# Performance work log

Measured on AMD Instinct MI355X. Metric: run time of the kernel, lower is better.

Reference implementation:

```python
import jax, jax.numpy as jnp
import numpy as np


def postorder_positions(depth):
    """Post-order index of each node in a perfect binary tree of given depth.
    Returns dict: level -> np.array of post-order indices for the left-to-right
    nodes at that level (level 0 = leaves, level `depth` = root)."""
    levels = {0: np.array([0], dtype=np.int64)}
    size = 1  # size of depth-(d-1) subtree
    for d in range(1, depth + 1):
        new = {l: np.concatenate([levels[l], levels[l] + size]) for l in range(d)}
        new[d] = np.array([2 * size], dtype=np.int64)
        levels = new
        size = 2 * size + 1
    return levels


def setup_inputs() -> dict:
    key = jax.random.key(0)
    k1, k2, k3, k4, k5, k6 = jax.random.split(key, 6)
    VOCAB, E, LBL, LEAVES = 50000, 100, 2, 131072  # 2**17 leaves
    word_ids = jax.random.randint(k1, (LEAVES,), 0, VOCAB, dtype=jnp.int32)
    emb_table = jax.random.normal(k2, (VOCAB, E), dtype=jnp.float32) * 0.1
    Wl = jax.random.normal(k3, (E, E), dtype=jnp.float32) * 0.1
    bl = jax.random.normal(k4, (E,), dtype=jnp.float32) * 0.1
    Wp = jax.random.normal(k5, (LBL, E), dtype=jnp.float32) * 0.1
    bp = jax.random.normal(k6, (LBL,), dtype=jnp.float32) * 0.1
    return {"word_ids": word_ids, "emb_table": emb_table, "Wl": Wl, "bl": bl, "Wp": Wp, "bp": bp}


def reference(word_ids, emb_table, Wl, bl, Wp, bp):
    # Perfect binary tree, batched level-by-level (same math as the per-node
    # Python recursion in the torch module). NOTE: original uses fcl for BOTH
    # children, so internal node = relu(fcl(left) + fcl(right)).
    L = word_ids.shape[0]
    D = int(round(np.log2(L)))
    pos = postorder_positions(D)
    n_nodes = 2 * L - 1

    h = emb_table[word_ids]  # [L, E] leaf states
    out = jnp.zeros((n_nodes, 1, bp.shape[0]), dtype=h.dtype)
    for lvl in range(D + 1):
        proj = h @ Wp.T + bp                     # [n_lvl, label]
        out = out.at[jnp.asarray(pos[lvl])].set(proj[:, None, :])
        if lvl < D:
            # fcl(left)+fcl(right) = (left+right) @ Wl^T + 2*bl, then relu
            h = jax.nn.relu((h[0::2] + h[1::2]) @ Wl.T + 2.0 * bl)
    return out  # [n_nodes, 1, label] in post-order, matching torch.cat(node_list)
```

## Files before the change

kernel.cpp:

```cpp
#include <hip/hip_runtime.h>

typedef _Float16 h8v __attribute__((ext_vector_type(8)));
typedef float f4v __attribute__((ext_vector_type(4)));

#define RS 136
#define SD 68

__device__ __forceinline__ unsigned pk2f(float a, float b) {
  unsigned short ha = __builtin_bit_cast(unsigned short, (_Float16)a);
  unsigned short hb = __builtin_bit_cast(unsigned short, (_Float16)b);
  return (unsigned)ha | ((unsigned)hb << 16);
}
__device__ __forceinline__ float2 upk(unsigned u) {
  _Float16 lo = __builtin_bit_cast(_Float16, (unsigned short)(u & 0xffffu));
  _Float16 hi = __builtin_bit_cast(_Float16, (unsigned short)(u >> 16));
  return make_float2((float)lo, (float)hi);
}

__global__ void prep_kernel(const float* __restrict__ Wl,
                            unsigned short* __restrict__ Wlf) {
  int i = blockIdx.x * 256 + threadIdx.x;
  if (i < 128 * 128) {
    int o = i >> 7, k = i & 127;
    _Float16 v = (_Float16)0.f;
    if (o < 100 && k < 100) v = (_Float16)Wl[o * 100 + k];
    Wlf[i] = __builtin_bit_cast(unsigned short, v);
  }
}

__device__ __forceinline__ void load_bfrags(
    const unsigned short* __restrict__ Wlf, const float* __restrict__ bl,
    h8v (&B0)[4], h8v (&B1)[4], float& bias0, float& bias1,
    int wave, int quad, int c16) {
  int col0 = wave * 32 + c16;
  int col1 = col0 + 16;
  bias0 = (col0 < 100) ? 2.0f * bl[col0] : 0.f;
  bias1 = (col1 < 100) ? 2.0f * bl[col1] : 0.f;
  const _Float16* w0 = (const _Float16*)Wlf + col0 * 128 + quad * 8;
  const _Float16* w1 = (const _Float16*)Wlf + col1 * 128 + quad * 8;
  B0[0] = *(const h8v*)(w0);      B0[1] = *(const h8v*)(w0 + 32);
  B0[2] = *(const h8v*)(w0 + 64); B0[3] = *(const h8v*)(w0 + 96);
  B1[0] = *(const h8v*)(w1);      B1[1] = *(const h8v*)(w1 + 32);
  B1[2] = *(const h8v*)(w1 + 64); B1[3] = *(const h8v*)(w1 + 96);
}

__device__ __forceinline__ void mfma_level(
    const _Float16* srcE, const _Float16* srcO, bool pairMode,
    _Float16* dstE, _Float16* dstO, int nOut,
    const h8v (&B0)[4], const h8v (&B1)[4], float bias0, float bias1,
    int lane, int wave) {
  const int quad = lane >> 4, c16 = lane & 15;
  const int col0 = wave * 32 + c16, col1 = col0 + 16;
  const int tiles = (nOut + 15) >> 4;
  for (int rt = 0; rt < tiles; ++rt) {
    const int r = rt * 16 + c16;
    const h8v* pe = (const h8v*)(srcE + (size_t)r * RS + quad * 8);
    h8v A0, A1, A2, A3;
    if (pairMode) {
      const h8v* po = (const h8v*)(srcO + (size_t)r * RS + quad * 8);
      A0 = pe[0] + po[0];  A1 = pe[4] + po[4];
      A2 = pe[8] + po[8];  A3 = pe[12] + po[12];
    } else {
      A0 = pe[0]; A1 = pe[4]; A2 = pe[8]; A3 = pe[12];
    }
    f4v a0 = {bias0, bias0, bias0, bias0};
    f4v a1 = {bias1, bias1, bias1, bias1};
    a0 = __builtin_amdgcn_mfma_f32_16x16x32_f16(A0, B0[0], a0, 0, 0, 0);
    a0 = __builtin_amdgcn_mfma_f32_16x16x32_f16(A1, B0[1], a0, 0, 0, 0);
    a0 = __builtin_amdgcn_mfma_f32_16x16x32_f16(A2, B0[2], a0, 0, 0, 0);
    a0 = __builtin_amdgcn_mfma_f32_16x16x32_f16(A3, B0[3], a0, 0, 0, 0);
    a1 = __builtin_amdgcn_mfma_f32_16x16x32_f16(A0, B1[0], a1, 0, 0, 0);
    a1 = __builtin_amdgcn_mfma_f32_16x16x32_f16(A1, B1[1], a1, 0, 0, 0);
    a1 = __builtin_amdgcn_mfma_f32_16x16x32_f16(A2, B1[2], a1, 0, 0, 0);
    a1 = __builtin_amdgcn_mfma_f32_16x16x32_f16(A3, B1[3], a1, 0, 0, 0);
    #pragma unroll
    for (int rg = 0; rg < 4; ++rg) {
      int row = rt * 16 + quad * 4 + rg;
      _Float16* dr = ((row & 1) ? dstO : dstE) + (size_t)(row >> 1) * RS;
      dr[col0] = (_Float16)fmaxf(a0[rg], 0.f);
      dr[col1] = (_Float16)fmaxf(a1[rg], 0.f);
    }
  }
}

__device__ __forceinline__ void proj_rows(
    const _Float16* E, const _Float16* O, int nRows, const float* WpS,
    float bp0, float bp1, int lvl, long gbase, float* __restrict__ out, int tid) {
  if (tid >= nRows) return;
  const unsigned* row = (const unsigned*)((tid & 1) ? O : E) + (size_t)(tid >> 1) * SD;
  float q0 = bp0, q1 = bp1;
  #pragma unroll
  for (int p = 0; p < 25; ++p) {
    uint2 u = ((const uint2*)row)[p];
    float2 a = upk(u.x), b = upk(u.y);
    q0 = fmaf(a.x, WpS[4*p], fmaf(a.y, WpS[4*p+1],
         fmaf(b.x, WpS[4*p+2], fmaf(b.y, WpS[4*p+3], q0))));
    q1 = fmaf(a.x, WpS[100+4*p], fmaf(a.y, WpS[100+4*p+1],
         fmaf(b.x, WpS[100+4*p+2], fmaf(b.y, WpS[100+4*p+3], q1))));
  }
  long g = gbase + tid;
  long pos = ((g + 1) << (lvl + 1)) - 2 - __popc((unsigned)g);
  out[2 * pos] = q0; out[2 * pos + 1] = q1;
}

__device__ void tree_phase(
    const unsigned* __restrict__ src, unsigned* __restrict__ hdst,
    _Float16* Ea, _Float16* Oa, _Float16* Eb, _Float16* Ob,
    const float* WpS, float bp0, float bp1,
    const h8v (&B0)[4], const h8v (&B1)[4], float bias0, float bias1,
    float* __restrict__ out, int firstLvl, int nLvl, int nIn, int finalProj,
    long blk, int tid, int lane, int wave) {
  {
    unsigned* Ed = (unsigned*)Ea; unsigned* Od = (unsigned*)Oa;
    for (int i = tid; i < 64 * 64; i += 256) {
      int r = i >> 6, d = i & 63;
      unsigned val = (r < nIn && d < 50) ? src[(size_t)r * 50 + d] : 0u;
      ((r & 1) ? Od : Ed)[(r >> 1) * SD + d] = val;
    }
    unsigned* Ed2 = (unsigned*)Eb; unsigned* Od2 = (unsigned*)Ob;
    for (int i = tid; i < 32 * 64; i += 256) {
      int r = i >> 6, d = i & 63;
      ((r & 1) ? Od2 : Ed2)[(r >> 1) * SD + d] = 0u;
    }
  }
  __syncthreads();
  _Float16 *sE = Ea, *sO = Oa, *dE = Eb, *dO = Ob;
  int n = nIn >> 1;
  for (int p = 0; p < nLvl; ++p) {
    mfma_level(sE, sO, true, dE, dO, n, B0, B1, bias0, bias1, lane, wave);
    proj_rows(sE, sO, n * 2, WpS, bp0, bp1, firstLvl + p - 1,
              blk * (n * 2), out, tid);
    __syncthreads();
    _Float16* t;
    t = sE; sE = dE; dE = t;
    t = sO; sO = dO; dO = t;
    n >>= 1;
  }
  int R = nIn >> nLvl;
  if (finalProj)
    proj_rows(sE, sO, R, WpS, bp0, bp1, firstLvl + nLvl - 1, blk * R, out, tid);
  if (hdst) {
    for (int i = tid; i < R * 50; i += 256) {
      int r = i / 50, d = i % 50;
      hdst[(size_t)blk * R * 50 + i] =
          ((const unsigned*)((r & 1) ? sO : sE))[(r >> 1) * SD + d];
    }
  }
  __syncthreads();
}

__global__ __launch_bounds__(256, 4) void mega_kernel(
    const int* __restrict__ word_ids, const float* __restrict__ emb,
    const unsigned short* __restrict__ Wlf, const float* __restrict__ bl,
    const float* __restrict__ Wp, const float* __restrict__ bp,
    unsigned* __restrict__ h7g, unsigned* __restrict__ h13g,
    unsigned* __restrict__ cnts, float* __restrict__ out) {
  __shared__ _Float16 S1[64 * RS];
  __shared__ _Float16 Ea[32 * RS], Oa[32 * RS];
  __shared__ float WpS[200];
  __shared__ int claimS;
  _Float16* const Eb = S1;
  _Float16* const Ob = S1 + 16 * RS;

  const int tid = threadIdx.x, lane = tid & 63;
  const int wave = __builtin_amdgcn_readfirstlane(tid >> 6);
  const int quad = lane >> 4, c16 = lane & 15;
  const int blk = blockIdx.x;

  if (tid < 200) WpS[tid] = Wp[tid];
  {
    unsigned* S1d = (unsigned*)S1;
    for (int i = tid; i < 64 * 14; i += 256) S1d[(i / 14) * SD + 50 + (i % 14)] = 0;
  }
  const float bp0 = bp[0], bp1 = bp[1];

  const int l = tid >> 1, hh = tid & 1;
  const long gL = (long)blk * 128 + l;
  const float4* row4 = (const float4*)(emb + (size_t)word_ids[gL] * 100);
  float4 v[13];
  #pragma unroll
  for (int i = 0; i < 13; ++i) {
    int q = 13 * hh + i;
    if (q < 25) v[i] = row4[q];
  }
  __syncthreads();

  {
    float q0 = 0.f, q1 = 0.f;
    #pragma unroll
    for (int i = 0; i < 13; ++i) {
      int q = 13 * hh + i;
      if (q < 25) {
        q0 = fmaf(v[i].x, WpS[4*q], fmaf(v[i].y, WpS[4*q+1],
             fmaf(v[i].z, WpS[4*q+2], fmaf(v[i].w, WpS[4*q+3], q0))));
        q1 = fmaf(v[i].x, WpS[100+4*q], fmaf(v[i].y, WpS[100+4*q+1],
             fmaf(v[i].z, WpS[100+4*q+2], fmaf(v[i].w, WpS[100+4*q+3], q1))));
      }
    }
    q0 += __shfl_xor(q0, 1, 64);
    q1 += __shfl_xor(q1, 1, 64);
    if (hh == 0) {
      long pos = ((gL + 1) << 1) - 2 - __popc((unsigned)gL);
      out[2 * pos] = q0 + bp0; out[2 * pos + 1] = q1 + bp1;
    }
  }
  {
    unsigned* S1d = (unsigned*)S1;
    #pragma unroll
    for (int i = 0; i < 13; ++i) {
      int q = 13 * hh + i;
      if (q < 25) {
        float sx = v[i].x + __shfl_xor(v[i].x, 2, 64);
        float sy = v[i].y + __shfl_xor(v[i].y, 2, 64);
        float sz = v[i].z + __shfl_xor(v[i].z, 2, 64);
        float sw = v[i].w + __shfl_xor(v[i].w, 2, 64);
        if ((tid & 2) == 0) {
          int m = tid >> 2;
          S1d[m * SD + 2*q]     = pk2f(sx, sy);
          S1d[m * SD + 2*q + 1] = pk2f(sz, sw);
        }
      }
    }
  }
  h8v B0[4], B1[4]; float bias0, bias1;
  load_bfrags(Wlf, bl, B0, B1, bias0, bias1, wave, quad, c16);
  __syncthreads();

  mfma_level(S1, nullptr, false, Ea, Oa, 64, B0, B1, bias0, bias1, lane, wave);
  __syncthreads();
  mfma_level(Ea, Oa, true, Eb, Ob, 32, B0, B1, bias0, bias1, lane, wave);
  proj_rows(Ea, Oa, 64, WpS, bp0, bp1, 1, (long)blk * 64, out, tid);
  __syncthreads();
  mfma_level(Eb, Ob, true, Ea, Oa, 16, B0, B1, bias0, bias1, lane, wave);
  proj_rows(Eb, Ob, 32, WpS, bp0, bp1, 2, (long)blk * 32, out, tid);
  __syncthreads();
  mfma_level(Ea, Oa, true, Eb, Ob, 8, B0, B1, bias0, bias1, lane, wave);
  proj_rows(Ea, Oa, 16, WpS, bp0, bp1, 3, (long)blk * 16, out, tid);
  __syncthreads();
  mfma_level(Eb, Ob, true, Ea, Oa, 4, B0, B1, bias0, bias1, lane, wave);
  proj_rows(Eb, Ob, 8, WpS, bp0, bp1, 4, (long)blk * 8, out, tid);
  __syncthreads();
  mfma_level(Ea, Oa, true, Eb, Ob, 2, B0, B1, bias0, bias1, lane, wave);
  proj_rows(Ea, Oa, 4, WpS, bp0, bp1, 5, (long)blk * 4, out, tid);
  __syncthreads();
  mfma_level(Eb, Ob, true, Ea, Oa, 1, B0, B1, bias0, bias1, lane, wave);
  proj_rows(Eb, Ob, 2, WpS, bp0, bp1, 6, (long)blk * 2, out, tid);
  __syncthreads();
  if (tid < 50) h7g[(size_t)blk * 50 + tid] = ((unsigned*)Ea)[tid];
  __syncthreads();

  const int g = blk >> 6;
  if (tid == 0) {
    __threadfence();
    unsigned old = atomicAdd(&cnts[g], 1u);
    int c = (old == 63u);
    if (c) __threadfence();
    claimS = c;
  }
  __syncthreads();
  if (!claimS) return;

  tree_phase(h7g + (size_t)g * 64 * 50, h13g, Ea, Oa, Eb, Ob, WpS, bp0, bp1,
             B0, B1, bias0, bias1, out, 8, 6, 64, 0, (long)g, tid, lane, wave);

  if (tid == 0) {
    __threadfence();
    unsigned old = atomicAdd(&cnts[16], 1u);
    int c = (old == 15u);
    if (c) __threadfence();
    claimS = c;
  }
  __syncthreads();
  if (!claimS) return;

  tree_phase(h13g, nullptr, Ea, Oa, Eb, Ob, WpS, bp0, bp1,
             B0, B1, bias0, bias1, out, 14, 4, 16, 1, 0L, tid, lane, wave);
}

extern "C" void kernel_launch(void* const* d_in, const int* in_sizes, int n_in,
                              void* d_out, int out_size, void* d_ws, size_t ws_size,
                              hipStream_t stream) {
  const int*   word_ids = (const int*)  d_in[0];
  const float* emb      = (const float*)d_in[1];
  const float* Wl       = (const float*)d_in[2];
  const float* bl       = (const float*)d_in[3];
  const float* Wp       = (const float*)d_in[4];
  const float* bp       = (const float*)d_in[5];
  float* out = (float*)d_out;

  unsigned short* Wlf = (unsigned short*)d_ws;
  unsigned* h7g  = (unsigned*)((char*)d_ws + 32768);
  unsigned* h13g = (unsigned*)((char*)d_ws + 32768 + 204800);
  unsigned* cnts = (unsigned*)((char*)d_ws + 32768 + 204800 + 3200);

  hipMemsetAsync(cnts, 0, 128, stream);
  prep_kernel<<<64, 256, 0, stream>>>(Wl, Wlf);
  mega_kernel<<<1024, 256, 0, stream>>>(word_ids, emb, Wlf, bl, Wp, bp,
                                        h7g, h13g, cnts, out);
}
```

Baseline: 159.9 us.

## Pre-convert embedding table to padded fp16 and precompute per-word leaf projections

The prep kernel now converts the whole embedding table to a 64-word padded fp16 layout and computes the leaf output projection once per vocabulary word. The main kernel then gathers half-size fp16 rows and reads the leaf projection directly, which cuts gather bytes and per-leaf arithmetic. In exchange the whole 50k-row table is converted on every call, even though only the gathered rows are used. Separately, the threadfences around the cross-block counters are replaced with relaxed agent-scope atomics, which weakens the memory-ordering guarantees for the tree hand-off.

```diff
diff --git a/kernel.cpp b/kernel.cpp
--- a/kernel.cpp
+++ b/kernel.cpp
@@ -17,14 +17,44 @@
   return make_float2((float)lo, (float)hi);
 }
 
-__global__ void prep_kernel(const float* __restrict__ Wl,
-                            unsigned short* __restrict__ Wlf) {
-  int i = blockIdx.x * 256 + threadIdx.x;
-  if (i < 128 * 128) {
-    int o = i >> 7, k = i & 127;
-    _Float16 v = (_Float16)0.f;
-    if (o < 100 && k < 100) v = (_Float16)Wl[o * 100 + k];
-    Wlf[i] = __builtin_bit_cast(unsigned short, v);
+__global__ void prep_kernel(const float* __restrict__ Wl, const float* __restrict__ emb,
+                            const float* __restrict__ Wp, const float* __restrict__ bp,
+                            unsigned short* __restrict__ Wlf, unsigned* __restrict__ embh,
+                            float2* __restrict__ pw) {
+  const long t = (long)blockIdx.x * 256 + threadIdx.x;
+  if (t < 100000L) {
+    const int w = (int)(t >> 1), hh = (int)(t & 1);
+    const float4* row4 = (const float4*)(emb + (size_t)w * 100);
+    unsigned* ed = embh + (size_t)w * 64;
+    float q0 = 0.f, q1 = 0.f;
+    #pragma unroll
+    for (int i = 0; i < 13; ++i) {
+      int q = 13 * hh + i;
+      if (q < 25) {
+        float4 v = row4[q];
+        q0 = fmaf(v.x, Wp[4*q], fmaf(v.y, Wp[4*q+1],
+             fmaf(v.z, Wp[4*q+2], fmaf(v.w, Wp[4*q+3], q0))));
+        q1 = fmaf(v.x, Wp[100+4*q], fmaf(v.y, Wp[100+4*q+1],
+             fmaf(v.z, Wp[100+4*q+2], fmaf(v.w, Wp[100+4*q+3], q1))));
+        ed[2*q]   = pk2f(v.x, v.y);
+        ed[2*q+1] = pk2f(v.z, v.w);
+      }
+    }
+    if (hh) {
+      #pragma unroll
+      for (int d = 50; d < 64; ++d) ed[d] = 0u;
+    }
+    q0 += __shfl_xor(q0, 1, 64);
+    q1 += __shfl_xor(q1, 1, 64);
+    if (!hh) pw[w] = make_float2(q0 + bp[0], q1 + bp[1]);
+  } else {
+    long j = t - 100096L;
+    if (j >= 0 && j < 128 * 128) {
+      int o = (int)(j >> 7), k = (int)(j & 127);
+      _Float16 v = (_Float16)0.f;
+      if (o < 100 && k < 100) v = (_Float16)Wl[o * 100 + k];
+      Wlf[j] = __builtin_bit_cast(unsigned short, v);
+    }
   }
 }
 
@@ -95,8 +125,8 @@
     float2 a = upk(u.x), b = upk(u.y);
     q0 = fmaf(a.x, WpS[4*p], fmaf(a.y, WpS[4*p+1],
          fmaf(b.x, WpS[4*p+2], fmaf(b.y, WpS[4*p+3], q0))));
-    q1 = fmaf(a.x, WpS[100+4*p], fmaf(a.y, WpS[100+4*p+1],
-         fmaf(b.x, WpS[100+4*p+2], fmaf(b.y, WpS[100+4*p+3], q1))));
+    q1 = fmaf(a.x, WpS[128+4*p], fmaf(a.y, WpS[128+4*p+1],
+         fmaf(b.x, WpS[128+4*p+2], fmaf(b.y, WpS[128+4*p+3], q1))));
   }
   long g = gbase + tid;
   long pos = ((g + 1) << (lvl + 1)) - 2 - __popc((unsigned)g);
@@ -114,7 +144,10 @@
     unsigned* Ed = (unsigned*)Ea; unsigned* Od = (unsigned*)Oa;
     for (int i = tid; i < 64 * 64; i += 256) {
       int r = i >> 6, d = i & 63;
-      unsigned val = (r < nIn && d < 50) ? src[(size_t)r * 50 + d] : 0u;
+      unsigned val = (r < nIn && d < 50)
+          ? __hip_atomic_load(&src[(size_t)r * 50 + d], __ATOMIC_RELAXED,
+                              __HIP_MEMORY_SCOPE_AGENT)
+          : 0u;
       ((r & 1) ? Od : Ed)[(r >> 1) * SD + d] = val;
     }
     unsigned* Ed2 = (unsigned*)Eb; unsigned* Od2 = (unsigned*)Ob;
@@ -142,22 +175,24 @@
   if (hdst) {
     for (int i = tid; i < R * 50; i += 256) {
       int r = i / 50, d = i % 50;
-      hdst[(size_t)blk * R * 50 + i] =
-          ((const unsigned*)((r & 1) ? sO : sE))[(r >> 1) * SD + d];
+      unsigned val = ((const unsigned*)((r & 1) ? sO : sE))[(r >> 1) * SD + d];
+      __hip_atomic_store(&hdst[(size_t)blk * R * 50 + i], val,
+                         __ATOMIC_RELAXED, __HIP_MEMORY_SCOPE_AGENT);
     }
   }
   __syncthreads();
 }
 
 __global__ __launch_bounds__(256, 4) void mega_kernel(
-    const int* __restrict__ word_ids, const float* __restrict__ emb,
+    const int* __restrict__ word_ids, const unsigned* __restrict__ embh,
+    const float2* __restrict__ pw,
     const unsigned short* __restrict__ Wlf, const float* __restrict__ bl,
     const float* __restrict__ Wp, const float* __restrict__ bp,
     unsigned* __restrict__ h7g, unsigned* __restrict__ h13g,
     unsigned* __restrict__ cnts, float* __restrict__ out) {
   __shared__ _Float16 S1[64 * RS];
   __shared__ _Float16 Ea[32 * RS], Oa[32 * RS];
-  __shared__ float WpS[200];
+  __shared__ float WpS[256];
   __shared__ int claimS;
   _Float16* const Eb = S1;
   _Float16* const Ob = S1 + 16 * RS;
@@ -167,59 +202,36 @@
   const int quad = lane >> 4, c16 = lane & 15;
   const int blk = blockIdx.x;
 
-  if (tid < 200) WpS[tid] = Wp[tid];
+  {
+    int r = tid >> 7, c = tid & 127;
+    WpS[tid] = (c < 100) ? Wp[r * 100 + c] : 0.f;
+  }
+  const float bp0 = bp[0], bp1 = bp[1];
+
+  const int l = tid >> 1, hh = tid & 1;
+  const long gL = (long)blk * 128 + l;
+  const int wid = word_ids[gL];
+  const uint4* erow = (const uint4*)(embh + (size_t)wid * 64 + hh * 32);
+  uint4 w4[8];
+  #pragma unroll
+  for (int i = 0; i < 8; ++i) w4[i] = erow[i];
+
+  if (hh == 0) {
+    float2 p = pw[wid];
+    long pos = ((gL + 1) << 1) - 2 - __popc((unsigned)gL);
+    out[2 * pos] = p.x; out[2 * pos + 1] = p.y;
+  }
+
   {
     unsigned* S1d = (unsigned*)S1;
-    for (int i = tid; i < 64 * 14; i += 256) S1d[(i / 14) * SD + 50 + (i % 14)] = 0;
-  }
-  const float bp0 = bp[0], bp1 = bp[1];
-
-  const int l = tid >> 1, hh = tid & 1;
-  const long gL = (long)blk * 128 + l;
-  const float4* row4 = (const float4*)(emb + (size_t)word_ids[gL] * 100);
-  float4 v[13];
-  #pragma unroll
-  for (int i = 0; i < 13; ++i) {
-    int q = 13 * hh + i;
-    if (q < 25) v[i] = row4[q];
-  }
-  __syncthreads();
-
-  {
-    float q0 = 0.f, q1 = 0.f;
+    const unsigned* wd = (const unsigned*)w4;
     #pragma unroll
-    for (int i = 0; i < 13; ++i) {
-      int q = 13 * hh + i;
-      if (q < 25) {
-        q0 = fmaf(v[i].x, WpS[4*q], fmaf(v[i].y, WpS[4*q+1],
-             fmaf(v[i].z, WpS[4*q+2], fmaf(v[i].w, WpS[4*q+3], q0))));
-        q1 = fmaf(v[i].x, WpS[100+4*q], fmaf(v[i].y, WpS[100+4*q+1],
-             fmaf(v[i].z, WpS[100+4*q+2], fmaf(v[i].w, WpS[100+4*q+3], q1))));
-      }
-    }
-    q0 += __shfl_xor(q0, 1, 64);
-    q1 += __shfl_xor(q1, 1, 64);
-    if (hh == 0) {
-      long pos = ((gL + 1) << 1) - 2 - __popc((unsigned)gL);
-      out[2 * pos] = q0 + bp0; out[2 * pos + 1] = q1 + bp1;
-    }
-  }
-  {
-    unsigned* S1d = (unsigned*)S1;
-    #pragma unroll
-    for (int i = 0; i < 13; ++i) {
-      int q = 13 * hh + i;
-      if (q < 25) {
-        float sx = v[i].x + __shfl_xor(v[i].x, 2, 64);
-        float sy = v[i].y + __shfl_xor(v[i].y, 2, 64);
-        float sz = v[i].z + __shfl_xor(v[i].z, 2, 64);
-        float sw = v[i].w + __shfl_xor(v[i].w, 2, 64);
-        if ((tid & 2) == 0) {
-          int m = tid >> 2;
-          S1d[m * SD + 2*q]     = pk2f(sx, sy);
-          S1d[m * SD + 2*q + 1] = pk2f(sz, sw);
-        }
-      }
+    for (int k = 0; k < 32; ++k) {
+      unsigned u = wd[k];
+      unsigned us = __shfl_xor(u, 2, 64);
+      float2 a = upk(u), b = upk(us);
+      unsigned pk = pk2f(a.x + b.x, a.y + b.y);
+      if ((tid & 2) == 0) S1d[(size_t)(tid >> 2) * SD + hh * 32 + k] = pk;
     }
   }
   h8v B0[4], B1[4]; float bias0, bias1;
@@ -246,16 +258,16 @@
   mfma_level(Eb, Ob, true, Ea, Oa, 1, B0, B1, bias0, bias1, lane, wave);
   proj_rows(Eb, Ob, 2, WpS, bp0, bp1, 6, (long)blk * 2, out, tid);
   __syncthreads();
-  if (tid < 50) h7g[(size_t)blk * 50 + tid] = ((unsigned*)Ea)[tid];
+  if (tid < 50)
+    __hip_atomic_store(&h7g[(size_t)blk * 50 + tid], ((unsigned*)Ea)[tid],
+                       __ATOMIC_RELAXED, __HIP_MEMORY_SCOPE_AGENT);
   __syncthreads();
 
   const int g = blk >> 6;
   if (tid == 0) {
-    __threadfence();
-    unsigned old = atomicAdd(&cnts[g], 1u);
-    int c = (old == 63u);
-    if (c) __threadfence();
-    claimS = c;
+    unsigned old = __hip_atomic_fetch_add(&cnts[g], 1u, __ATOMIC_RELAXED,
+                                          __HIP_MEMORY_SCOPE_AGENT);
+    claimS = (old == 63u);
   }
   __syncthreads();
   if (!claimS) return;
@@ -264,11 +276,9 @@
              B0, B1, bias0, bias1, out, 8, 6, 64, 0, (long)g, tid, lane, wave);
 
   if (tid == 0) {
-    __threadfence();
-    unsigned old = atomicAdd(&cnts[16], 1u);
-    int c = (old == 15u);
-    if (c) __threadfence();
-    claimS = c;
+    unsigned old = __hip_atomic_fetch_add(&cnts[16], 1u, __ATOMIC_RELAXED,
+                                          __HIP_MEMORY_SCOPE_AGENT);
+    claimS = (old == 15u);
   }
   __syncthreads();
   if (!claimS) return;
@@ -288,13 +298,15 @@
   const float* bp       = (const float*)d_in[5];
   float* out = (float*)d_out;
 
-  unsigned short* Wlf = (unsigned short*)d_ws;
-  unsigned* h7g  = (unsigned*)((char*)d_ws + 32768);
-  unsigned* h13g = (unsigned*)((char*)d_ws + 32768 + 204800);
-  unsigned* cnts = (unsigned*)((char*)d_ws + 32768 + 204800 + 3200);
+  unsigned*       embh = (unsigned*)d_ws;
+  float2*         pw   = (float2*)((char*)d_ws + 12800000);
+  unsigned short* Wlf  = (unsigned short*)((char*)d_ws + 13200000);
+  unsigned*       h7g  = (unsigned*)((char*)d_ws + 13232768);
+  unsigned*       h13g = (unsigned*)((char*)d_ws + 13437568);
+  unsigned*       cnts = (unsigned*)((char*)d_ws + 13440768);
 
   hipMemsetAsync(cnts, 0, 128, stream);
-  prep_kernel<<<64, 256, 0, stream>>>(Wl, Wlf);
-  mega_kernel<<<1024, 256, 0, stream>>>(word_ids, emb, Wlf, bl, Wp, bp,
+  prep_kernel<<<455, 256, 0, stream>>>(Wl, emb, Wp, bp, Wlf, embh, pw);
+  mega_kernel<<<1024, 256, 0, stream>>>(word_ids, embh, pw, Wlf, bl, Wp, bp,
                                         h7g, h13g, cnts, out);
 }
```

Result: faster. 153.6 us (-3.9%).
